# Optimization experiments

Measured on AMD Instinct MI355X. Metric: run time of the kernel, lower is better.

The kernel has to match this reference:

```python
import jax, jax.numpy as jnp
import numpy as np

B, L, V = 64, 32, 16000
ENC, DEC, ATT, EMB = 512, 512, 512, 256
H = W = 16

def setup_inputs() -> dict:
    key = jax.random.key(0)
    ks = jax.random.split(key, 24)
    def lin(k, out_d, in_d):
        s = 1.0 / np.sqrt(in_d)
        k1, k2 = jax.random.split(k)
        return (jax.random.uniform(k1, (out_d, in_d), jnp.float32, -s, s),
                jax.random.uniform(k2, (out_d,), jnp.float32, -s, s))
    encoder_out = jax.random.normal(ks[0], (B, ENC, H, W), jnp.float32)
    encoded_captions = jax.random.randint(ks[1], (B, L), 0, V)
    lens = jax.random.randint(ks[2], (B,), 2, L + 1)
    lens = jnp.sort(lens)[::-1].at[0].set(L)  # sorted descending, max = L
    W_enc_att, b_enc_att = lin(ks[3], ATT, ENC)
    W_dec_att, b_dec_att = lin(ks[4], ATT, DEC)
    w_full, b_full = lin(ks[5], 1, ATT)
    emb = jax.random.normal(ks[6], (V, EMB), jnp.float32)
    s = 1.0 / np.sqrt(DEC)
    W_ih = jax.random.uniform(ks[7], (4 * DEC, EMB + ENC), jnp.float32, -s, s)
    W_hh = jax.random.uniform(ks[8], (4 * DEC, DEC), jnp.float32, -s, s)
    b_ih = jax.random.uniform(ks[9], (4 * DEC,), jnp.float32, -s, s)
    b_hh = jax.random.uniform(ks[10], (4 * DEC,), jnp.float32, -s, s)
    W_init_h, b_init_h = lin(ks[11], DEC, ENC)
    W_init_c, b_init_c = lin(ks[12], DEC, ENC)
    W_beta, b_beta = lin(ks[13], ENC, DEC)
    W_fc, b_fc = lin(ks[14], V, DEC)
    return dict(encoder_out=encoder_out, encoded_captions=encoded_captions,
                caption_lengths=lens,
                W_enc_att=W_enc_att, b_enc_att=b_enc_att,
                W_dec_att=W_dec_att, b_dec_att=b_dec_att,
                w_full=w_full, b_full=b_full, emb=emb,
                W_ih=W_ih, W_hh=W_hh, b_ih=b_ih, b_hh=b_hh,
                W_init_h=W_init_h, b_init_h=b_init_h,
                W_init_c=W_init_c, b_init_c=b_init_c,
                W_beta=W_beta, b_beta=b_beta, W_fc=W_fc, b_fc=b_fc)

def reference(encoder_out, encoded_captions, caption_lengths,
              W_enc_att, b_enc_att, W_dec_att, b_dec_att, w_full, b_full, emb,
              W_ih, W_hh, b_ih, b_hh, W_init_h, b_init_h, W_init_c, b_init_c,
              W_beta, b_beta, W_fc, b_fc):
    # encoder_out: [B, C, H, W] -> [B, P, C]
    enc = jnp.transpose(encoder_out, (0, 2, 3, 1)).reshape(encoder_out.shape[0], -1, ENC)
    emb_seq = emb[encoded_captions]                      # [B, L, E]
    mean_enc = enc.mean(axis=1)
    h0 = mean_enc @ W_init_h.T + b_init_h
    c0 = mean_enc @ W_init_c.T + b_init_c
    att1 = enc @ W_enc_att.T + b_enc_att                 # [B, P, A] (time-invariant)
    T = encoded_captions.shape[1] - 1                    # static max(decode_lengths)
    dl = caption_lengths - 1
    masks = jnp.arange(T)[:, None] < dl[None, :]         # [T, B]
    xs = (jnp.swapaxes(emb_seq[:, :T, :], 0, 1), masks)  # ([T,B,E], [T,B])

    def step(carry, x):
        h, c = carry
        emb_t, mask = x
        att2 = h @ W_dec_att.T + b_dec_att               # [B, A]
        e = jnp.einsum('bpa,a->bp', jax.nn.relu(att1 + att2[:, None, :]), w_full[0]) + b_full[0]
        alpha = jax.nn.softmax(e, axis=1)                # [B, P]
        awe = jnp.einsum('bpc,bp->bc', enc, alpha)       # [B, ENC]
        gate = jax.nn.sigmoid(h @ W_beta.T + b_beta)
        awe = gate * awe
        xin = jnp.concatenate([emb_t, awe], axis=1)      # [B, E+ENC]
        gates = xin @ W_ih.T + b_ih + h @ W_hh.T + b_hh  # [B, 4*DEC]
        i, f, g, o = jnp.split(gates, 4, axis=1)
        c2 = jax.nn.sigmoid(f) * c + jax.nn.sigmoid(i) * jnp.tanh(g)
        h2 = jax.nn.sigmoid(o) * jnp.tanh(c2)
        pred = h2 @ W_fc.T + b_fc                        # dropout in eval mode = identity
        pred = jnp.where(mask[:, None], pred, 0.0)       # inactive rows stay zero
        return (h2, c2), pred

    (_, _), preds = jax.lax.scan(step, (h0, c0), xs)     # [T, B, V]
    return jnp.swapaxes(preds, 0, 1)                     # [B, T, V]
```

## Files before the change

### kernel.cpp

```cpp
#include <hip/hip_runtime.h>

#define BB   64
#define LL   32
#define TT   31
#define VV   16000
#define PP   256
#define CE   512
#define CD   512
#define CA   512
#define CEMB 256
#define G4   2048

typedef unsigned short u16;

struct alignas(16) u16x8 { u16 v[8]; };

__device__ __forceinline__ float bf2f(u16 u){
  union { unsigned int i; float f; } x; x.i = ((unsigned int)u) << 16; return x.f;
}
__device__ __forceinline__ u16 f2bf(float f){
  union { float f; unsigned int i; } x; x.f = f;
  unsigned int r = x.i + 0x7fffu + ((x.i >> 16) & 1u);
  return (u16)(r >> 16);
}
__device__ __forceinline__ float sigm(float x){ return 1.0f/(1.0f + __expf(-x)); }

__global__ void k_detect(const int* __restrict__ lens32, int* __restrict__ flag){
  if (threadIdx.x == 0 && blockIdx.x == 0) flag[0] = (lens32[1] == 0) ? 1 : 0;
}


__global__ __launch_bounds__(256) void k_mean(const float* __restrict__ eo,
                                              float* __restrict__ mean_enc){
  int i = blockIdx.x*256 + threadIdx.x;
  const float4* row = (const float4*)(eo + (size_t)i*PP);
  float s = 0.f;
  for (int j = 0; j < PP/4; j++){
    float4 w = row[j];
    s += w.x + w.y + w.z + w.w;
  }
  mean_enc[i] = s * (1.0f/PP);
}

__global__ __launch_bounds__(256) void k_trans(const float* __restrict__ eo,
                                               float* __restrict__ eoT){
  __shared__ float T[64][65];
  int b = blockIdx.z, c0 = blockIdx.x*64, p0 = blockIdx.y*64;
  int tid = threadIdx.x;
  int lx = tid & 63, ly = tid >> 6;
  #pragma unroll
  for (int r = 0; r < 16; r++){
    int c = ly + 4*r;
    T[c][lx] = eo[((size_t)b*CE + c0 + c)*PP + p0 + lx];
  }
  __syncthreads();
  #pragma unroll
  for (int r = 0; r < 16; r++){
    int p = ly + 4*r;
    eoT[((size_t)b*PP + p0 + p)*CE + c0 + lx] = T[lx][p];
  }
}

__global__ __launch_bounds__(256) void k_init(const float* __restrict__ mean_enc,
    const float* __restrict__ Wh, const float* __restrict__ bh,
    const float* __restrict__ Wc, const float* __restrict__ bc,
    float* __restrict__ h, float* __restrict__ c){
  __shared__ float ms[CE];
  int b = blockIdx.x >> 1, half = blockIdx.x & 1;
  int tid = threadIdx.x;
  ms[tid]       = mean_enc[b*CE + tid];
  ms[tid + 256] = mean_enc[b*CE + 256 + tid];
  __syncthreads();
  int d = half*256 + tid;
  const float4* wh = (const float4*)(Wh + (size_t)d*CE);
  const float4* wc = (const float4*)(Wc + (size_t)d*CE);
  float ah = 0.f, ac = 0.f;
  for (int k4 = 0; k4 < CE/4; k4++){
    float4 a = wh[k4], bq = wc[k4];
    float m0 = ms[k4*4+0], m1 = ms[k4*4+1], m2 = ms[k4*4+2], m3 = ms[k4*4+3];
    ah = fmaf(m0,a.x, fmaf(m1,a.y, fmaf(m2,a.z, fmaf(m3,a.w, ah))));
    ac = fmaf(m0,bq.x,fmaf(m1,bq.y,fmaf(m2,bq.z,fmaf(m3,bq.w, ac))));
  }
  h[b*CD + d] = ah + bh[d];
  c[b*CD + d] = ac + bc[d];
}

__global__ __launch_bounds__(256) void k_emb(const int* __restrict__ caps,
                                             const float* __restrict__ emb,
                                             float* __restrict__ eseq,
                                             const int* __restrict__ flag){
  int i = blockIdx.x*256 + threadIdx.x;
  if (i >= BB*TT*CEMB/4) return;
  int flat = i*4;
  int b = flat / (TT*CEMB);
  int r = flat % (TT*CEMB);
  int t = r / CEMB;
  int e = r % CEMB;
  int li = b*LL + t;
  int tok = flag[0] ? caps[2*li] : caps[li];
  tok = tok < 0 ? 0 : (tok >= VV ? VV-1 : tok);
  *(float4*)(eseq + flat) = *(const float4*)(emb + (size_t)tok*CEMB + e);
}

__global__ __launch_bounds__(256) void k_att1(const float* __restrict__ eo,
    const float* __restrict__ W, const float* __restrict__ bias,
    u16* __restrict__ att1){
  __shared__ float As[16][132];
  __shared__ float Bs[16][132];
  int b  = blockIdx.z;
  int p0 = blockIdx.y * 128;
  int a0 = blockIdx.x * 128;
  int tid = threadIdx.x;
  int ty = tid >> 4, tx = tid & 15;
  float acc[8][8] = {};
  int lk  = tid >> 4;
  int lm  = (tid & 15) * 8;
  int ln  = tid >> 1;
  int lkb = (tid & 1) * 8;
  for (int c0 = 0; c0 < CE; c0 += 16){
    __syncthreads();
    const float* ap = eo + ((size_t)b*CE + c0 + lk)*PP + p0 + lm;
    float4 av0 = *(const float4*)ap;
    float4 av1 = *(const float4*)(ap + 4);
    As[lk][lm+0]=av0.x; As[lk][lm+1]=av0.y; As[lk][lm+2]=av0.z; As[lk][lm+3]=av0.w;
    As[lk][lm+4]=av1.x; As[lk][lm+5]=av1.y; As[lk][lm+6]=av1.z; As[lk][lm+7]=av1.w;
    const float* bp = W + (size_t)(a0 + ln)*CE + c0 + lkb;
    float4 bw0 = *(const float4*)bp;
    float4 bw1 = *(const float4*)(bp + 4);
    Bs[lkb+0][ln]=bw0.x; Bs[lkb+1][ln]=bw0.y; Bs[lkb+2][ln]=bw0.z; Bs[lkb+3][ln]=bw0.w;
    Bs[lkb+4][ln]=bw1.x; Bs[lkb+5][ln]=bw1.y; Bs[lkb+6][ln]=bw1.z; Bs[lkb+7][ln]=bw1.w;
    __syncthreads();
    #pragma unroll
    for (int k = 0; k < 16; k++){
      float4 a0v = *(const float4*)&As[k][ty*8];
      float4 a1v = *(const float4*)&As[k][ty*8 + 4];
      float4 b0v = *(const float4*)&Bs[k][tx*8];
      float4 b1v = *(const float4*)&Bs[k][tx*8 + 4];
      float a[8]  = {a0v.x,a0v.y,a0v.z,a0v.w,a1v.x,a1v.y,a1v.z,a1v.w};
      float bb[8] = {b0v.x,b0v.y,b0v.z,b0v.w,b1v.x,b1v.y,b1v.z,b1v.w};
      #pragma unroll
      for (int i2 = 0; i2 < 8; i2++)
        #pragma unroll
        for (int j2 = 0; j2 < 8; j2++)
          acc[i2][j2] = fmaf(a[i2], bb[j2], acc[i2][j2]);
    }
  }
  float bv[8];
  #pragma unroll
  for (int j2 = 0; j2 < 8; j2++) bv[j2] = bias[a0 + tx*8 + j2];
  #pragma unroll
  for (int i2 = 0; i2 < 8; i2++){
    int p = p0 + ty*8 + i2;
    u16x8 o;
    #pragma unroll
    for (int j2 = 0; j2 < 8; j2++) o.v[j2] = f2bf(acc[i2][j2] + bv[j2]);
    *(u16x8*)(att1 + ((size_t)(b*PP + p))*CA + a0 + tx*8) = o;
  }
}


__global__ __launch_bounds__(256) void k_pre(
    const float* __restrict__ h, const float* __restrict__ eseq,
    const float* __restrict__ Wda, const float* __restrict__ Wbe,
    const float* __restrict__ Wih, const float* __restrict__ Whh,
    float* __restrict__ att2slab, float* __restrict__ gslab, int t){
  __shared__ float As[16][68];
  __shared__ float Bs[16][68];
  int blk = blockIdx.x, tid = threadIdx.x;
  int ty = tid >> 4, tx = tid & 15;
  int lb  = tid >> 2;
  int lk4 = (tid & 3) * 4;
  int ln  = tid >> 2;
  int lkb = (tid & 3) * 4;
  if (blk < 32){
    int jblk = blk & 15, kc = blk >> 4;
    int n0 = jblk * 64;
    const float* W = (n0 < 512) ? Wda : Wbe;
    int rowbase = (n0 < 512) ? n0 : (n0 - 512);
    float acc[4][4] = {};
    for (int k0 = 0; k0 < 256; k0 += 16){
      __syncthreads();
      float4 q = *(const float4*)(h + (size_t)lb*CD + kc*256 + k0 + lk4);
      As[lk4+0][lb] = q.x; As[lk4+1][lb] = q.y; As[lk4+2][lb] = q.z; As[lk4+3][lb] = q.w;
      float4 w4 = *(const float4*)(W + (size_t)(rowbase + ln)*CD + kc*256 + k0 + lkb);
      Bs[lkb+0][ln] = w4.x; Bs[lkb+1][ln] = w4.y; Bs[lkb+2][ln] = w4.z; Bs[lkb+3][ln] = w4.w;
      __syncthreads();
      #pragma unroll
      for (int k = 0; k < 16; k++){
        float4 av = *(const float4*)&As[k][ty*4];
        float4 bv = *(const float4*)&Bs[k][tx*4];
        float a[4] = {av.x, av.y, av.z, av.w};
        float bq[4] = {bv.x, bv.y, bv.z, bv.w};
        #pragma unroll
        for (int i2 = 0; i2 < 4; i2++)
          #pragma unroll
          for (int j2 = 0; j2 < 4; j2++)
            acc[i2][j2] = fmaf(a[i2], bq[j2], acc[i2][j2]);
      }
    }
    #pragma unroll
    for (int i2 = 0; i2 < 4; i2++){
      int bq = ty*4 + i2;
      float4 o = make_float4(acc[i2][0], acc[i2][1], acc[i2][2], acc[i2][3]);
      *(float4*)(att2slab + ((size_t)(kc*BB + bq))*1024 + n0 + tx*4) = o;
    }
  } else {
    int local = blk - 32;
    int chunk = (local < 32) ? 0 : ((local < 64) ? 3 : 4);
    int jblk = local & 31;
    int j0 = jblk * 64;
    const float* Wbase; int wrow, wcol0;
    if (chunk == 0){ Wbase = Wih; wrow = 768; wcol0 = 0; }
    else           { Wbase = Whh; wrow = 512; wcol0 = (chunk - 3) * 256; }
    float acc[4][4] = {};
    for (int k0 = 0; k0 < 256; k0 += 16){
      __syncthreads();
      const float* src;
      if (chunk == 0) src = eseq + ((size_t)lb*TT + t)*CEMB;
      else            src = h    + (size_t)lb*CD + (chunk - 3)*256;
      float4 q = *(const float4*)(src + k0 + lk4);
      As[lk4+0][lb] = q.x; As[lk4+1][lb] = q.y; As[lk4+2][lb] = q.z; As[lk4+3][lb] = q.w;
      float4 w4 = *(const float4*)(Wbase + (size_t)(j0 + ln)*wrow + wcol0 + k0 + lkb);
      Bs[lkb+0][ln] = w4.x; Bs[lkb+1][ln] = w4.y; Bs[lkb+2][ln] = w4.z; Bs[lkb+3][ln] = w4.w;
      __syncthreads();
      #pragma unroll
      for (int k = 0; k < 16; k++){
        float4 av = *(const float4*)&As[k][ty*4];
        float4 bv = *(const float4*)&Bs[k][tx*4];
        float a[4] = {av.x, av.y, av.z, av.w};
        float bq[4] = {bv.x, bv.y, bv.z, bv.w};
        #pragma unroll
        for (int i2 = 0; i2 < 4; i2++)
          #pragma unroll
          for (int j2 = 0; j2 < 4; j2++)
            acc[i2][j2] = fmaf(a[i2], bq[j2], acc[i2][j2]);
      }
    }
    #pragma unroll
    for (int i2 = 0; i2 < 4; i2++){
      int bq = ty*4 + i2;
      float4 o = make_float4(acc[i2][0], acc[i2][1], acc[i2][2], acc[i2][3]);
      *(float4*)(gslab + ((size_t)chunk*BB + bq)*G4 + j0 + tx*4) = o;
    }
  }
}

__global__ __launch_bounds__(256) void k_attsm(
    const float* __restrict__ att2slab,
    const float* __restrict__ bd, const float* __restrict__ bb_,
    const float* __restrict__ wfull, const float* __restrict__ bfull,
    const u16* __restrict__ att1, const float* __restrict__ eoT,
    float* __restrict__ awe){
  __shared__ float att2s[CA];
  __shared__ float gs[CE];
  __shared__ float wl[CA];
  __shared__ float es[PP];
  __shared__ float red[8];
  int b = blockIdx.x, tid = threadIdx.x;
  wl[tid]       = wfull[tid];
  wl[tid + 256] = wfull[256 + tid];
  {
    const float* s0 = att2slab + (size_t)b*1024;
    const float* s1 = att2slab + (size_t)(BB + b)*1024;
    att2s[tid]       = s0[tid]       + s1[tid]       + bd[tid];
    att2s[tid + 256] = s0[tid + 256] + s1[tid + 256] + bd[tid + 256];
    float2 g0 = *(const float2*)(s0 + 512 + 2*tid);
    float2 g1 = *(const float2*)(s1 + 512 + 2*tid);
    float2 bbv = *(const float2*)(bb_ + 2*tid);
    gs[2*tid]     = sigm(g0.x + g1.x + bbv.x);
    gs[2*tid + 1] = sigm(g0.y + g1.y + bbv.y);
  }
  __syncthreads();
  float e;
  {
    const u16x8* ar = (const u16x8*)(att1 + ((size_t)(b*PP + tid))*CA);
    float s = 0.f;
    for (int k8 = 0; k8 < CA/8; k8++){
      u16x8 a8 = ar[k8];
      #pragma unroll
      for (int q = 0; q < 8; q++){
        float v = bf2f(a8.v[q]) + att2s[k8*8 + q];
        s = fmaf(fmaxf(v, 0.f), wl[k8*8 + q], s);
      }
    }
    e = s + bfull[0];
  }
  int lane = tid & 63, wid = tid >> 6;
  float v = e;
  #pragma unroll
  for (int off = 32; off; off >>= 1) v = fmaxf(v, __shfl_xor(v, off, 64));
  if (lane == 0) red[wid] = v;
  __syncthreads();
  float mx = fmaxf(fmaxf(red[0], red[1]), fmaxf(red[2], red[3]));
  float ex = __expf(e - mx);
  float sm = ex;
  #pragma unroll
  for (int off = 32; off; off >>= 1) sm += __shfl_xor(sm, off, 64);
  if (lane == 0) red[4 + wid] = sm;
  __syncthreads();
  float tot = red[4] + red[5] + red[6] + red[7];
  es[tid] = ex / tot;
  __syncthreads();
  {
    const float* base = eoT + (size_t)b*PP*CE + 2*tid;
    float s0 = 0.f, s1 = 0.f;
    #pragma unroll 4
    for (int p = 0; p < PP; p++){
      float2 v2 = *(const float2*)(base + (size_t)p*CE);
      float a = es[p];
      s0 = fmaf(v2.x, a, s0);
      s1 = fmaf(v2.y, a, s1);
    }
    float2 o = make_float2(s0 * gs[2*tid], s1 * gs[2*tid + 1]);
    *(float2*)(awe + b*CE + 2*tid) = o;
  }
}

__global__ __launch_bounds__(256) void k_gl(
    const float* __restrict__ awe, const float* __restrict__ Wih,
    const float* __restrict__ gslab,
    const float* __restrict__ bih, const float* __restrict__ bhh,
    float* __restrict__ h, float* __restrict__ c,
    float* __restrict__ h_all, int t){
  __shared__ float awe_s[16][68];
  __shared__ float W_s[16][20];
  int blk = blockIdx.x, tid = threadIdx.x;
  int d0 = blk * 4;
  int bq = tid & 63, cq = tid >> 6;
  int lb  = tid >> 2;
  int lk4 = (tid & 3) * 4;
  float4 acc = make_float4(0.f, 0.f, 0.f, 0.f);
  for (int k0 = 0; k0 < 512; k0 += 16){
    __syncthreads();
    float4 q = *(const float4*)(awe + (size_t)lb*CE + k0 + lk4);
    awe_s[lk4+0][lb] = q.x; awe_s[lk4+1][lb] = q.y;
    awe_s[lk4+2][lb] = q.z; awe_s[lk4+3][lb] = q.w;
    if (tid < 64){
      int ln = tid >> 2;
      int gi2 = ln & 3, di2 = ln >> 2;
      int grow = gi2*512 + d0 + di2;
      float4 w4 = *(const float4*)(Wih + (size_t)grow*768 + 256 + k0 + lk4);
      W_s[lk4+0][ln] = w4.x; W_s[lk4+1][ln] = w4.y;
      W_s[lk4+2][ln] = w4.z; W_s[lk4+3][ln] = w4.w;
    }
    __syncthreads();
    #pragma unroll
    for (int k = 0; k < 16; k++){
      float a = awe_s[k][bq];
      float4 w = *(const float4*)&W_s[k][cq*4];
      acc.x = fmaf(a, w.x, acc.x);
      acc.y = fmaf(a, w.y, acc.y);
      acc.z = fmaf(a, w.z, acc.z);
      acc.w = fmaf(a, w.w, acc.w);
    }
  }
  int d = d0 + cq;
  float gi = acc.x + bih[d]        + bhh[d];
  float gf = acc.y + bih[d + 512]  + bhh[d + 512];
  float gg = acc.z + bih[d + 1024] + bhh[d + 1024];
  float go = acc.w + bih[d + 1536] + bhh[d + 1536];
  #pragma unroll
  for (int s = 0; s < 5; s += 1){
    if (s == 1 || s == 2) continue;
    const float* base = gslab + ((size_t)s*BB + bq)*G4;
    gi += base[d]; gf += base[d + 512]; gg += base[d + 1024]; go += base[d + 1536];
  }
  int i = bq*CD + d;
  float cn = sigm(gf)*c[i] + sigm(gi)*tanhf(gg);
  float hn = sigm(go)*tanhf(cn);
  c[i] = cn; h[i] = hn;
  h_all[((size_t)bq*TT + t)*CD + d] = hn;
}

__global__ __launch_bounds__(256) void k_pred(
    const float* __restrict__ h_all, const float* __restrict__ Wfc,
    const float* __restrict__ bfc, const int* __restrict__ lens,
    const int* __restrict__ flag, float* __restrict__ out){
  __shared__ float As[16][132];
  __shared__ float Bs[16][132];
  int n0 = blockIdx.x * 128;
  int m0 = blockIdx.y * 128;
  int tid = threadIdx.x;
  int ty = tid >> 4, tx = tid & 15;
  float acc[8][8] = {};
  int lm  = tid >> 1;
  int lkb = (tid & 1) * 8;
  for (int c0 = 0; c0 < CD; c0 += 16){
    __syncthreads();
    int m = m0 + lm;
    float4 a0v, a1v;
    if (m < BB*TT){
      a0v = *(const float4*)(h_all + (size_t)m*CD + c0 + lkb);
      a1v = *(const float4*)(h_all + (size_t)m*CD + c0 + lkb + 4);
    } else {
      a0v = make_float4(0.f,0.f,0.f,0.f); a1v = a0v;
    }
    As[lkb+0][lm] = a0v.x; As[lkb+1][lm] = a0v.y; As[lkb+2][lm] = a0v.z; As[lkb+3][lm] = a0v.w;
    As[lkb+4][lm] = a1v.x; As[lkb+5][lm] = a1v.y; As[lkb+6][lm] = a1v.z; As[lkb+7][lm] = a1v.w;
    const float* bp = Wfc + (size_t)(n0 + lm)*CD + c0 + lkb;
    float4 b0v = *(const float4*)bp;
    float4 b1v = *(const float4*)(bp + 4);
    Bs[lkb+0][lm] = b0v.x; Bs[lkb+1][lm] = b0v.y; Bs[lkb+2][lm] = b0v.z; Bs[lkb+3][lm] = b0v.w;
    Bs[lkb+4][lm] = b1v.x; Bs[lkb+5][lm] = b1v.y; Bs[lkb+6][lm] = b1v.z; Bs[lkb+7][lm] = b1v.w;
    __syncthreads();
    #pragma unroll
    for (int k = 0; k < 16; k++){
      float4 av0 = *(const float4*)&As[k][ty*8];
      float4 av1 = *(const float4*)&As[k][ty*8 + 4];
      float4 bv0 = *(const float4*)&Bs[k][tx*8];
      float4 bv1 = *(const float4*)&Bs[k][tx*8 + 4];
      float a[8]  = {av0.x,av0.y,av0.z,av0.w,av1.x,av1.y,av1.z,av1.w};
      float bb[8] = {bv0.x,bv0.y,bv0.z,bv0.w,bv1.x,bv1.y,bv1.z,bv1.w};
      #pragma unroll
      for (int i2 = 0; i2 < 8; i2++)
        #pragma unroll
        for (int j2 = 0; j2 < 8; j2++)
          acc[i2][j2] = fmaf(a[i2], bb[j2], acc[i2][j2]);
    }
  }
  float bv[8];
  #pragma unroll
  for (int j2 = 0; j2 < 8; j2++) bv[j2] = bfc[n0 + tx*8 + j2];
  int f = flag[0];
  #pragma unroll
  for (int i2 = 0; i2 < 8; i2++){
    int m = m0 + ty*8 + i2;
    if (m < BB*TT){
      int b = m / TT, t = m - b*TT;
      int lb = f ? lens[2*b] : lens[b];
      bool active = (t < lb - 1);
      float4 o0, o1;
      if (active){
        o0 = make_float4(acc[i2][0]+bv[0], acc[i2][1]+bv[1], acc[i2][2]+bv[2], acc[i2][3]+bv[3]);
        o1 = make_float4(acc[i2][4]+bv[4], acc[i2][5]+bv[5], acc[i2][6]+bv[6], acc[i2][7]+bv[7]);
      } else {
        o0 = make_float4(0.f,0.f,0.f,0.f); o1 = o0;
      }
      float* op = out + (size_t)m*VV + n0 + tx*8;
      *(float4*)op       = o0;
      *(float4*)(op + 4) = o1;
    }
  }
}

extern "C" void kernel_launch(void* const* d_in, const int* in_sizes, int n_in,
                              void* d_out, int out_size, void* d_ws, size_t ws_size,
                              hipStream_t stream){
  const float* eo    = (const float*)d_in[0];
  const int*   caps  = (const int*)d_in[1];
  const int*   lens  = (const int*)d_in[2];
  const float* Wea   = (const float*)d_in[3];
  const float* bea   = (const float*)d_in[4];
  const float* Wda   = (const float*)d_in[5];
  const float* bda   = (const float*)d_in[6];
  const float* wfull = (const float*)d_in[7];
  const float* bfull = (const float*)d_in[8];
  const float* emb   = (const float*)d_in[9];
  const float* Wih   = (const float*)d_in[10];
  const float* Whh   = (const float*)d_in[11];
  const float* bih   = (const float*)d_in[12];
  const float* bhh   = (const float*)d_in[13];
  const float* Wirh  = (const float*)d_in[14];
  const float* birh  = (const float*)d_in[15];
  const float* Wirc  = (const float*)d_in[16];
  const float* birc  = (const float*)d_in[17];
  const float* Wbe   = (const float*)d_in[18];
  const float* bbe   = (const float*)d_in[19];
  const float* Wfc   = (const float*)d_in[20];
  const float* bfc   = (const float*)d_in[21];
  float* out = (float*)d_out;

  char* ob = (char*)d_out;
  u16*   att1     = (u16*)(ob + 0);
  float* gslab    = (float*)(ob + 16777216);
  float* eseq     = (float*)(ob + 19398656);
  float* mean_enc = (float*)(ob + 21430272);
  float* awe      = (float*)(ob + 21561344);
  float* hbuf     = (float*)(ob + 21692416);
  float* cbuf     = (float*)(ob + 21823488);
  float* att2slab = (float*)(ob + 21954560);
  float* eoT      = (float*)(ob + 22478848);
  char* w = (char*)d_ws;
  float* h_all    = (float*)w;
  int*   iflag    = (int*)(w + 4063232);

  k_detect<<<1, 64, 0, stream>>>(lens, iflag);
  k_mean<<<128, 256, 0, stream>>>(eo, mean_enc);
  k_trans<<<dim3(8, 4, BB), 256, 0, stream>>>(eo, eoT);
  k_emb <<<496, 256, 0, stream>>>(caps, emb, eseq, iflag);
  k_init<<<128, 256, 0, stream>>>(mean_enc, Wirh, birh, Wirc, birc, hbuf, cbuf);
  k_att1<<<dim3(4, 2, BB), 256, 0, stream>>>(eo, Wea, bea, att1);
  for (int t = 0; t < TT; t++){
    k_pre  <<<128, 256, 0, stream>>>(hbuf, eseq, Wda, Wbe, Wih, Whh, att2slab, gslab, t);
    k_attsm<<<BB, 256, 0, stream>>>(att2slab, bda, bbe, wfull, bfull, att1, eoT, awe);
    k_gl   <<<128, 256, 0, stream>>>(awe, Wih, gslab, bih, bhh, hbuf, cbuf, h_all, t);
  }
  k_pred<<<dim3(125, 16), 256, 0, stream>>>(h_all, Wfc, bfc, lens, iflag, out);
}
```

Measured before the change: 3.227 ms.

## Fuse per-timestep recurrent kernels into one persistent cooperative kernel with grid syncs

The 93 separate launches of the pre, attention-softmax and gate/LSTM kernels are replaced by a single cooperative kernel of 128 blocks. It loops over timesteps and places grid.sync() between the phases, with a shared-memory union so each phase reuses the same LDS. The aim is to remove per-launch overhead and inter-kernel gaps on the serial recurrence. In exchange it adds grid-wide barrier cost, and only 64 of the 128 blocks are active during the attention phase.

```diff
diff --git a/kernel.cpp b/kernel.cpp
--- a/kernel.cpp
+++ b/kernel.cpp
@@ -1,4 +1,7 @@
 #include <hip/hip_runtime.h>
+#include <hip/hip_cooperative_groups.h>
+
+namespace cg = cooperative_groups;
 
 #define BB   64
 #define LL   32
@@ -159,14 +162,17 @@
 }
 
 
-__global__ __launch_bounds__(256) void k_pre(
+union SharedU {
+  struct { float As[16][68], Bs[16][68]; } pre;
+  struct { float att2s[CA], gs[CE], wl[CA], es[PP], red[8]; } att;
+  struct { float awe_s[16][68], W_s[16][20]; } gl;
+};
+
+__device__ __forceinline__ void pre_body(int blk, int tid, SharedU& S,
     const float* __restrict__ h, const float* __restrict__ eseq,
     const float* __restrict__ Wda, const float* __restrict__ Wbe,
     const float* __restrict__ Wih, const float* __restrict__ Whh,
     float* __restrict__ att2slab, float* __restrict__ gslab, int t){
-  __shared__ float As[16][68];
-  __shared__ float Bs[16][68];
-  int blk = blockIdx.x, tid = threadIdx.x;
   int ty = tid >> 4, tx = tid & 15;
   int lb  = tid >> 2;
   int lk4 = (tid & 3) * 4;
@@ -181,14 +187,16 @@
     for (int k0 = 0; k0 < 256; k0 += 16){
       __syncthreads();
       float4 q = *(const float4*)(h + (size_t)lb*CD + kc*256 + k0 + lk4);
-      As[lk4+0][lb] = q.x; As[lk4+1][lb] = q.y; As[lk4+2][lb] = q.z; As[lk4+3][lb] = q.w;
+      S.pre.As[lk4+0][lb] = q.x; S.pre.As[lk4+1][lb] = q.y;
+      S.pre.As[lk4+2][lb] = q.z; S.pre.As[lk4+3][lb] = q.w;
       float4 w4 = *(const float4*)(W + (size_t)(rowbase + ln)*CD + kc*256 + k0 + lkb);
-      Bs[lkb+0][ln] = w4.x; Bs[lkb+1][ln] = w4.y; Bs[lkb+2][ln] = w4.z; Bs[lkb+3][ln] = w4.w;
+      S.pre.Bs[lkb+0][ln] = w4.x; S.pre.Bs[lkb+1][ln] = w4.y;
+      S.pre.Bs[lkb+2][ln] = w4.z; S.pre.Bs[lkb+3][ln] = w4.w;
       __syncthreads();
       #pragma unroll
       for (int k = 0; k < 16; k++){
-        float4 av = *(const float4*)&As[k][ty*4];
-        float4 bv = *(const float4*)&Bs[k][tx*4];
+        float4 av = *(const float4*)&S.pre.As[k][ty*4];
+        float4 bv = *(const float4*)&S.pre.Bs[k][tx*4];
         float a[4] = {av.x, av.y, av.z, av.w};
         float bq[4] = {bv.x, bv.y, bv.z, bv.w};
         #pragma unroll
@@ -219,14 +227,16 @@
       if (chunk == 0) src = eseq + ((size_t)lb*TT + t)*CEMB;
       else            src = h    + (size_t)lb*CD + (chunk - 3)*256;
       float4 q = *(const float4*)(src + k0 + lk4);
-      As[lk4+0][lb] = q.x; As[lk4+1][lb] = q.y; As[lk4+2][lb] = q.z; As[lk4+3][lb] = q.w;
+      S.pre.As[lk4+0][lb] = q.x; S.pre.As[lk4+1][lb] = q.y;
+      S.pre.As[lk4+2][lb] = q.z; S.pre.As[lk4+3][lb] = q.w;
       float4 w4 = *(const float4*)(Wbase + (size_t)(j0 + ln)*wrow + wcol0 + k0 + lkb);
-      Bs[lkb+0][ln] = w4.x; Bs[lkb+1][ln] = w4.y; Bs[lkb+2][ln] = w4.z; Bs[lkb+3][ln] = w4.w;
+      S.pre.Bs[lkb+0][ln] = w4.x; S.pre.Bs[lkb+1][ln] = w4.y;
+      S.pre.Bs[lkb+2][ln] = w4.z; S.pre.Bs[lkb+3][ln] = w4.w;
       __syncthreads();
       #pragma unroll
       for (int k = 0; k < 16; k++){
-        float4 av = *(const float4*)&As[k][ty*4];
-        float4 bv = *(const float4*)&Bs[k][tx*4];
+        float4 av = *(const float4*)&S.pre.As[k][ty*4];
+        float4 bv = *(const float4*)&S.pre.Bs[k][tx*4];
         float a[4] = {av.x, av.y, av.z, av.w};
         float bq[4] = {bv.x, bv.y, bv.z, bv.w};
         #pragma unroll
@@ -245,18 +255,17 @@
   }
 }
 
-__global__ __launch_bounds__(256) void k_attsm(
+__device__ __forceinline__ void attsm_body(int b, int tid, SharedU& S,
     const float* __restrict__ att2slab,
     const float* __restrict__ bd, const float* __restrict__ bb_,
     const float* __restrict__ wfull, const float* __restrict__ bfull,
     const u16* __restrict__ att1, const float* __restrict__ eoT,
     float* __restrict__ awe){
-  __shared__ float att2s[CA];
-  __shared__ float gs[CE];
-  __shared__ float wl[CA];
-  __shared__ float es[PP];
-  __shared__ float red[8];
-  int b = blockIdx.x, tid = threadIdx.x;
+  float* att2s = S.att.att2s;
+  float* gs    = S.att.gs;
+  float* wl    = S.att.wl;
+  float* es    = S.att.es;
+  float* red   = S.att.red;
   wl[tid]       = wfull[tid];
   wl[tid + 256] = wfull[256 + tid];
   {
@@ -316,15 +325,12 @@
   }
 }
 
-__global__ __launch_bounds__(256) void k_gl(
+__device__ __forceinline__ void gl_body(int blk, int tid, SharedU& S,
     const float* __restrict__ awe, const float* __restrict__ Wih,
     const float* __restrict__ gslab,
     const float* __restrict__ bih, const float* __restrict__ bhh,
     float* __restrict__ h, float* __restrict__ c,
     float* __restrict__ h_all, int t){
-  __shared__ float awe_s[16][68];
-  __shared__ float W_s[16][20];
-  int blk = blockIdx.x, tid = threadIdx.x;
   int d0 = blk * 4;
   int bq = tid & 63, cq = tid >> 6;
   int lb  = tid >> 2;
@@ -333,21 +339,21 @@
   for (int k0 = 0; k0 < 512; k0 += 16){
     __syncthreads();
     float4 q = *(const float4*)(awe + (size_t)lb*CE + k0 + lk4);
-    awe_s[lk4+0][lb] = q.x; awe_s[lk4+1][lb] = q.y;
-    awe_s[lk4+2][lb] = q.z; awe_s[lk4+3][lb] = q.w;
+    S.gl.awe_s[lk4+0][lb] = q.x; S.gl.awe_s[lk4+1][lb] = q.y;
+    S.gl.awe_s[lk4+2][lb] = q.z; S.gl.awe_s[lk4+3][lb] = q.w;
     if (tid < 64){
       int ln = tid >> 2;
       int gi2 = ln & 3, di2 = ln >> 2;
       int grow = gi2*512 + d0 + di2;
       float4 w4 = *(const float4*)(Wih + (size_t)grow*768 + 256 + k0 + lk4);
-      W_s[lk4+0][ln] = w4.x; W_s[lk4+1][ln] = w4.y;
-      W_s[lk4+2][ln] = w4.z; W_s[lk4+3][ln] = w4.w;
+      S.gl.W_s[lk4+0][ln] = w4.x; S.gl.W_s[lk4+1][ln] = w4.y;
+      S.gl.W_s[lk4+2][ln] = w4.z; S.gl.W_s[lk4+3][ln] = w4.w;
     }
     __syncthreads();
     #pragma unroll
     for (int k = 0; k < 16; k++){
-      float a = awe_s[k][bq];
-      float4 w = *(const float4*)&W_s[k][cq*4];
+      float a = S.gl.awe_s[k][bq];
+      float4 w = *(const float4*)&S.gl.W_s[k][cq*4];
       acc.x = fmaf(a, w.x, acc.x);
       acc.y = fmaf(a, w.y, acc.y);
       acc.z = fmaf(a, w.z, acc.z);
@@ -370,6 +376,32 @@
   float hn = sigm(go)*tanhf(cn);
   c[i] = cn; h[i] = hn;
   h_all[((size_t)bq*TT + t)*CD + d] = hn;
+}
+
+__global__ __launch_bounds__(256) void k_loop(
+    const float* __restrict__ eseq, const u16* __restrict__ att1,
+    const float* __restrict__ eoT,
+    const float* __restrict__ Wda, const float* __restrict__ bda,
+    const float* __restrict__ Wbe, const float* __restrict__ bbe,
+    const float* __restrict__ wfull, const float* __restrict__ bfull,
+    const float* __restrict__ Wih, const float* __restrict__ Whh,
+    const float* __restrict__ bih, const float* __restrict__ bhh,
+    float* __restrict__ hbuf, float* __restrict__ cbuf,
+    float* __restrict__ awe, float* __restrict__ gslab,
+    float* __restrict__ att2slab, float* __restrict__ h_all){
+  cg::grid_group grid = cg::this_grid();
+  __shared__ SharedU S;
+  int blk = blockIdx.x, tid = threadIdx.x;
+  for (int t = 0; t < TT; t++){
+    pre_body(blk, tid, S, hbuf, eseq, Wda, Wbe, Wih, Whh, att2slab, gslab, t);
+    grid.sync();
+    if (blk < 64){
+      attsm_body(blk, tid, S, att2slab, bda, bbe, wfull, bfull, att1, eoT, awe);
+    }
+    grid.sync();
+    gl_body(blk, tid, S, awe, Wih, gslab, bih, bhh, hbuf, cbuf, h_all, t);
+    grid.sync();
+  }
 }
 
 __global__ __launch_bounds__(256) void k_pred(
@@ -490,10 +522,19 @@
   k_emb <<<496, 256, 0, stream>>>(caps, emb, eseq, iflag);
   k_init<<<128, 256, 0, stream>>>(mean_enc, Wirh, birh, Wirc, birc, hbuf, cbuf);
   k_att1<<<dim3(4, 2, BB), 256, 0, stream>>>(eo, Wea, bea, att1);
-  for (int t = 0; t < TT; t++){
-    k_pre  <<<128, 256, 0, stream>>>(hbuf, eseq, Wda, Wbe, Wih, Whh, att2slab, gslab, t);
-    k_attsm<<<BB, 256, 0, stream>>>(att2slab, bda, bbe, wfull, bfull, att1, eoT, awe);
-    k_gl   <<<128, 256, 0, stream>>>(awe, Wih, gslab, bih, bhh, hbuf, cbuf, h_all, t);
-  }
+
+  {
+    void* kargs[] = {
+      (void*)&eseq, (void*)&att1, (void*)&eoT,
+      (void*)&Wda, (void*)&bda, (void*)&Wbe, (void*)&bbe,
+      (void*)&wfull, (void*)&bfull, (void*)&Wih, (void*)&Whh,
+      (void*)&bih, (void*)&bhh,
+      (void*)&hbuf, (void*)&cbuf, (void*)&awe, (void*)&gslab,
+      (void*)&att2slab, (void*)&h_all
+    };
+    hipLaunchCooperativeKernel(reinterpret_cast<void*>(k_loop),
+                               dim3(128), dim3(256), kargs, 0, stream);
+  }
+
   k_pred<<<dim3(125, 16), 256, 0, stream>>>(h_all, Wfc, bfc, lens, iflag, out);
 }
```

Measured after the change: 4.932 ms. +52.8%, slower.
